# Performance work log

Measured on AMD Instinct MI355X. Metric: run time of the kernel, lower is better.

## Reference

```python
import jax, jax.numpy as jnp
import numpy as np

BLOCK_SIZE = 32
BITS = 4
Q_MAX = 2 ** (BITS - 1) - 1  # 7


def setup_inputs() -> dict:
    key = jax.random.key(0)
    k1, k2, k3, k4 = jax.random.split(key, 4)
    B, S, D_in, D_out = 4, 2048, 4096, 4096
    x = jax.random.normal(k1, (B, S, D_in), dtype=jnp.float32)
    # 4-bit symmetric quantized values in [-8, 7], stored as int32
    weight_q = jax.random.randint(k2, (D_out, D_in), -(2 ** (BITS - 1)), 2 ** (BITS - 1), dtype=jnp.int32)
    # per-block positive scales (abs-max of each block in the original)
    block_scales = jax.random.uniform(k3, (D_out, D_in // BLOCK_SIZE), dtype=jnp.float32, minval=0.01, maxval=1.0)
    bias = jax.random.normal(k4, (D_out,), dtype=jnp.float32) * 0.01
    return {"x": x, "weight_q": weight_q, "block_scales": block_scales, "bias": bias}


def _dequantize(weight_q, block_scales):
    out_f, in_f = weight_q.shape
    n_blocks = in_f // BLOCK_SIZE
    q = weight_q.reshape(out_f, n_blocks, BLOCK_SIZE).astype(jnp.float32)
    w = q / Q_MAX * block_scales[:, :, None]
    return w.reshape(out_f, in_f)


def reference(x, weight_q, block_scales, bias):
    # block dequantize: w = q / q_max * scale, then y = x @ w.T + b
    w = _dequantize(weight_q, block_scales)  # [out, in] fp32
    return jnp.einsum('bsi,oi->bso', x, w) + bias
```

## Files before the change

kernel.cpp:

```cpp
#include <hip/hip_runtime.h>
#include <stdint.h>

#define M_DIM 8192
#define N_DIM 4096
#define K_DIM 4096
#define NBLK  (K_DIM / 32)

typedef __attribute__((ext_vector_type(4))) float          f32x4;
typedef __attribute__((ext_vector_type(8))) short          bf16x8;
typedef __attribute__((ext_vector_type(4))) int            i32x4;
typedef __attribute__((ext_vector_type(8))) unsigned short u16x8;

__device__ __forceinline__ unsigned short f2bf(float f) {
  unsigned u = __builtin_bit_cast(unsigned, f);
  u += 0x7fffu + ((u >> 16) & 1u);
  return (unsigned short)(u >> 16);
}

__device__ __forceinline__ void gload_lds16(const unsigned short* g, unsigned short* l) {
  __builtin_amdgcn_global_load_lds(
      (const __attribute__((address_space(1))) void*)g,
      (__attribute__((address_space(3))) void*)l, 16, 0, 0);
}

__global__ void MXFP4_dequant_kernel(const int* __restrict__ wq,
                                     const float* __restrict__ scales,
                                     unsigned short* __restrict__ wb) {
  int t = blockIdx.x * 256 + threadIdx.x;
  long e = (long)t * 8;
  int o = t >> 9;
  int k = (t & 511) << 3;
  float s = scales[o * NBLK + (k >> 5)] * (1.0f / 7.0f);
  i32x4 q0 = *(const i32x4*)(wq + e);
  i32x4 q1 = *(const i32x4*)(wq + e + 4);
  u16x8 r;
#pragma unroll
  for (int j = 0; j < 4; ++j) r[j]     = f2bf((float)q0[j] * s);
#pragma unroll
  for (int j = 0; j < 4; ++j) r[4 + j] = f2bf((float)q1[j] * s);
  *(u16x8*)(wb + e) = r;
}

__global__ void MXFP4_cvt_kernel(const float* __restrict__ x,
                                 unsigned short* __restrict__ xb) {
  long t = (long)blockIdx.x * 256 + threadIdx.x;
  long e = t * 8;
  f32x4 v0 = *(const f32x4*)(x + e);
  f32x4 v1 = *(const f32x4*)(x + e + 4);
  u16x8 r;
#pragma unroll
  for (int j = 0; j < 4; ++j) r[j]     = f2bf(v0[j]);
#pragma unroll
  for (int j = 0; j < 4; ++j) r[4 + j] = f2bf(v1[j]);
  *(u16x8*)(xb + e) = r;
}

__global__ __launch_bounds__(256, 2) void MXFP4_gemm_kernel(
    const unsigned short* __restrict__ A,
    const unsigned short* __restrict__ B,
    const float* __restrict__ bias,
    float* __restrict__ C) {
  __shared__ unsigned short As[128 * 32];
  __shared__ unsigned short Bs[128 * 32];

  const int tid  = threadIdx.x;
  const int lane = tid & 63;
  const int wave = tid >> 6;
  const int brow = blockIdx.y * 128;
  const int bcol = blockIdx.x * 128;
  const int wm   = (wave >> 1) * 64;
  const int wn   = (wave & 1) * 64;

  const int r0 = tid >> 2;
  const int c0 = (tid & 3) * 8;
  const unsigned short* ag0 = A + (long)(brow + r0) * K_DIM + c0;
  const unsigned short* ag1 = A + (long)(brow + r0 + 64) * K_DIM + c0;
  const unsigned short* bg0 = B + (long)(bcol + r0) * K_DIM + c0;
  const unsigned short* bg1 = B + (long)(bcol + r0 + 64) * K_DIM + c0;
  unsigned short* as0 = As + tid * 8;
  unsigned short* as1 = As + 2048 + tid * 8;
  unsigned short* bs0 = Bs + tid * 8;
  unsigned short* bs1 = Bs + 2048 + tid * 8;

  f32x4 acc[4][4] = {};

  const int fr = lane & 15;
  const int kc = (lane >> 4) * 8;

  for (int kt = 0; kt < K_DIM / 32; ++kt) {
    gload_lds16(ag0, as0);
    gload_lds16(ag1, as1);
    gload_lds16(bg0, bs0);
    gload_lds16(bg1, bs1);
    ag0 += 32; ag1 += 32; bg0 += 32; bg1 += 32;
    __syncthreads();

    bf16x8 af[4], bfr[4];
#pragma unroll
    for (int m = 0; m < 4; ++m)
      af[m] = *(const bf16x8*)(As + (wm + m * 16 + fr) * 32 + kc);
#pragma unroll
    for (int n = 0; n < 4; ++n)
      bfr[n] = *(const bf16x8*)(Bs + (wn + n * 16 + fr) * 32 + kc);
#pragma unroll
    for (int m = 0; m < 4; ++m)
#pragma unroll
      for (int n = 0; n < 4; ++n)
        acc[m][n] = __builtin_amdgcn_mfma_f32_16x16x32_bf16(af[m], bfr[n], acc[m][n], 0, 0, 0);
    __syncthreads();
  }

  const int rbase = brow + wm + (lane >> 4) * 4;
  const int cn    = lane & 15;
#pragma unroll
  for (int n = 0; n < 4; ++n) {
    int col  = bcol + wn + n * 16 + cn;
    float bv = bias[col];
#pragma unroll
    for (int m = 0; m < 4; ++m) {
      int row = rbase + m * 16;
#pragma unroll
      for (int j = 0; j < 4; ++j)
        C[(long)(row + j) * N_DIM + col] = acc[m][n][j] + bv;
    }
  }
}

extern "C" void kernel_launch(void* const* d_in, const int* in_sizes, int n_in,
                              void* d_out, int out_size, void* d_ws, size_t ws_size,
                              hipStream_t stream) {
  const float* x      = (const float*)d_in[0];
  const int*   wq     = (const int*)d_in[1];
  const float* scales = (const float*)d_in[2];
  const float* bias   = (const float*)d_in[3];
  float*       out    = (float*)d_out;

  unsigned short* wb = (unsigned short*)d_ws;
  unsigned short* xb = wb + (size_t)N_DIM * K_DIM;

  MXFP4_dequant_kernel<<<(N_DIM * (long)K_DIM / 8) / 256, 256, 0, stream>>>(wq, scales, wb);
  MXFP4_cvt_kernel<<<(M_DIM * (long)K_DIM / 8) / 256, 256, 0, stream>>>(x, xb);

  dim3 grid(N_DIM / 128, M_DIM / 128);
  MXFP4_gemm_kernel<<<grid, 256, 0, stream>>>(xb, wb, bias, out);
}
```

Before: 365.3 us.

## Rewrite GEMM as 256x256 tile, 8-wave double-buffered pipeline with swizzled grid

Replaces the 128x128 single-buffered bf16 GEMM with a 256x256 tile computed by 512 threads. K steps of 64 are double-buffered in LDS, with global-to-LDS staging interleaved between MFMA quarter-groups, explicit ds_read_b128 via inline asm, manual waitcnt/barrier control and s_setprio around MFMA bursts. The block index is also swizzled for L2 locality. The aim is to hide load latency and raise data reuse per LDS byte, at the cost of more registers, about 130 KB of LDS, and fragile hand-tuned vmcnt accounting.

```diff
diff --git a/kernel.cpp b/kernel.cpp
--- a/kernel.cpp
+++ b/kernel.cpp
@@ -10,6 +10,7 @@
 typedef __attribute__((ext_vector_type(8))) short          bf16x8;
 typedef __attribute__((ext_vector_type(4))) int            i32x4;
 typedef __attribute__((ext_vector_type(8))) unsigned short u16x8;
+typedef __attribute__((address_space(3))) unsigned short   lds_us;
 
 __device__ __forceinline__ unsigned short f2bf(float f) {
   unsigned u = __builtin_bit_cast(unsigned, f);
@@ -17,10 +18,17 @@
   return (unsigned short)(u >> 16);
 }
 
-__device__ __forceinline__ void gload_lds16(const unsigned short* g, unsigned short* l) {
+__device__ __forceinline__ void stage16(const unsigned short* g, lds_us* l) {
   __builtin_amdgcn_global_load_lds(
       (const __attribute__((address_space(1))) void*)g,
       (__attribute__((address_space(3))) void*)l, 16, 0, 0);
+}
+
+template <int OFF>
+__device__ __forceinline__ bf16x8 dsr(lds_us* addr) {
+  bf16x8 d;
+  asm volatile("ds_read_b128 %0, %1 offset:%2" : "=v"(d) : "v"(addr), "n"(OFF));
+  return d;
 }
 
 __global__ void MXFP4_dequant_kernel(const int* __restrict__ wq,
@@ -55,73 +63,139 @@
   *(u16x8*)(xb + e) = r;
 }
 
-__global__ __launch_bounds__(256, 2) void MXFP4_gemm_kernel(
+
+#define BAR() __builtin_amdgcn_s_barrier()
+#define WAIT_LGKM0() do { asm volatile("s_waitcnt lgkmcnt(0)" ::: "memory"); \
+                          __builtin_amdgcn_sched_barrier(0); } while (0)
+
+#define ST_A(t_, h_, BUFA_, valid_) do { \
+  if (valid_) { \
+    const unsigned short* s_ = srcA + (size_t)(h_) * 128 * K_DIM + (t_) * 64; \
+    lds_us* d_ = lp + (BUFA_) * 16384 + ((h_) * 8 + wv) * 1024; \
+    stage16(s_, d_); stage16(s_ + 32, d_ + 512); \
+  } else { stage16(srcA, lp + 65536); stage16(srcA + 32, lp + 65536 + 512); } \
+} while (0)
+
+#define ST_B(t_, h_, BUFB_, valid_) do { \
+  if (valid_) { \
+    const unsigned short* s_ = srcB + (size_t)(h_) * 128 * K_DIM + (t_) * 64; \
+    lds_us* d_ = lp + 32768 + (BUFB_) * 16384 + ((h_) * 8 + wv) * 1024; \
+    stage16(s_, d_); stage16(s_ + 32, d_ + 512); \
+  } else { stage16(srcB, lp + 65536); stage16(srcB + 32, lp + 65536 + 512); } \
+} while (0)
+
+#define MF(MB_, NB_, AF_, BF_) do { \
+  _Pragma("unroll") \
+  for (int kk_ = 0; kk_ < 2; ++kk_) \
+    _Pragma("unroll") \
+    for (int mm_ = 0; mm_ < 4; ++mm_) \
+      _Pragma("unroll") \
+      for (int nn_ = 0; nn_ < 2; ++nn_) \
+        acc[(MB_) + mm_][(NB_) + nn_] = __builtin_amdgcn_mfma_f32_16x16x32_bf16( \
+            AF_[mm_][kk_], BF_[nn_][kk_], acc[(MB_) + mm_][(NB_) + nn_], 0, 0, 0); \
+} while (0)
+
+#define GROUP(BUF_, tB_, tA_, vB_, vA_) do { \
+  lds_us* dsA_ = lp + (BUF_) * 16384 + wm * 8192 + lane * 8; \
+  lds_us* dsB_ = lp + 32768 + (BUF_) * 16384 + wn * 4096 + lane * 8; \
+   \
+  aLo[0][0] = dsr<0>(dsA_);      aLo[0][1] = dsr<1024>(dsA_); \
+  aLo[1][0] = dsr<2048>(dsA_);   aLo[1][1] = dsr<3072>(dsA_); \
+  aLo[2][0] = dsr<4096>(dsA_);   aLo[2][1] = dsr<5120>(dsA_); \
+  aLo[3][0] = dsr<6144>(dsA_);   aLo[3][1] = dsr<7168>(dsA_); \
+  bLo[0][0] = dsr<0>(dsB_);      bLo[0][1] = dsr<1024>(dsB_); \
+  bLo[1][0] = dsr<2048>(dsB_);   bLo[1][1] = dsr<3072>(dsB_); \
+  ST_B(tB_, 0, (BUF_) ^ 1, vB_); \
+  BAR(); WAIT_LGKM0(); \
+  __builtin_amdgcn_s_setprio(1); \
+  MF(0, 0, aLo, bLo); \
+  __builtin_amdgcn_s_setprio(0); \
+  BAR(); \
+   \
+  aHi[0][0] = dsr<8192>(dsA_);   aHi[0][1] = dsr<9216>(dsA_); \
+  aHi[1][0] = dsr<10240>(dsA_);  aHi[1][1] = dsr<11264>(dsA_); \
+  aHi[2][0] = dsr<12288>(dsA_);  aHi[2][1] = dsr<13312>(dsA_); \
+  aHi[3][0] = dsr<14336>(dsA_);  aHi[3][1] = dsr<15360>(dsA_); \
+  ST_B(tB_, 1, (BUF_) ^ 1, vB_); \
+  BAR(); WAIT_LGKM0(); \
+  __builtin_amdgcn_s_setprio(1); \
+  MF(4, 0, aHi, bLo); \
+  __builtin_amdgcn_s_setprio(0); \
+  BAR(); \
+   \
+  bHi[0][0] = dsr<4096>(dsB_);   bHi[0][1] = dsr<5120>(dsB_); \
+  bHi[1][0] = dsr<6144>(dsB_);   bHi[1][1] = dsr<7168>(dsB_); \
+  ST_A(tA_, 0, (BUF_), vA_); \
+  BAR(); WAIT_LGKM0(); \
+  __builtin_amdgcn_s_setprio(1); \
+  MF(0, 2, aLo, bHi); \
+  __builtin_amdgcn_s_setprio(0); \
+  BAR(); \
+   \
+  ST_A(tA_, 1, (BUF_), vA_); \
+  asm volatile("s_waitcnt vmcnt(4)" ::: "memory"); \
+  BAR(); \
+  __builtin_amdgcn_s_setprio(1); \
+  MF(4, 2, aHi, bHi); \
+  __builtin_amdgcn_s_setprio(0); \
+  BAR(); \
+} while (0)
+
+__global__ __launch_bounds__(512, 2) void MXFP4_gemm_kernel(
     const unsigned short* __restrict__ A,
     const unsigned short* __restrict__ B,
     const float* __restrict__ bias,
     float* __restrict__ C) {
-  __shared__ unsigned short As[128 * 32];
-  __shared__ unsigned short Bs[128 * 32];
+  __shared__ unsigned short LDS[66560];
+  lds_us* lp = (lds_us*)LDS;
 
   const int tid  = threadIdx.x;
   const int lane = tid & 63;
-  const int wave = tid >> 6;
-  const int brow = blockIdx.y * 128;
-  const int bcol = blockIdx.x * 128;
-  const int wm   = (wave >> 1) * 64;
-  const int wn   = (wave & 1) * 64;
-
-  const int r0 = tid >> 2;
-  const int c0 = (tid & 3) * 8;
-  const unsigned short* ag0 = A + (long)(brow + r0) * K_DIM + c0;
-  const unsigned short* ag1 = A + (long)(brow + r0 + 64) * K_DIM + c0;
-  const unsigned short* bg0 = B + (long)(bcol + r0) * K_DIM + c0;
-  const unsigned short* bg1 = B + (long)(bcol + r0 + 64) * K_DIM + c0;
-  unsigned short* as0 = As + tid * 8;
-  unsigned short* as1 = As + 2048 + tid * 8;
-  unsigned short* bs0 = Bs + tid * 8;
-  unsigned short* bs1 = Bs + 2048 + tid * 8;
-
-  f32x4 acc[4][4] = {};
-
-  const int fr = lane & 15;
-  const int kc = (lane >> 4) * 8;
-
-  for (int kt = 0; kt < K_DIM / 32; ++kt) {
-    gload_lds16(ag0, as0);
-    gload_lds16(ag1, as1);
-    gload_lds16(bg0, bs0);
-    gload_lds16(bg1, bs1);
-    ag0 += 32; ag1 += 32; bg0 += 32; bg1 += 32;
-    __syncthreads();
-
-    bf16x8 af[4], bfr[4];
-#pragma unroll
-    for (int m = 0; m < 4; ++m)
-      af[m] = *(const bf16x8*)(As + (wm + m * 16 + fr) * 32 + kc);
-#pragma unroll
-    for (int n = 0; n < 4; ++n)
-      bfr[n] = *(const bf16x8*)(Bs + (wn + n * 16 + fr) * 32 + kc);
-#pragma unroll
-    for (int m = 0; m < 4; ++m)
-#pragma unroll
-      for (int n = 0; n < 4; ++n)
-        acc[m][n] = __builtin_amdgcn_mfma_f32_16x16x32_bf16(af[m], bfr[n], acc[m][n], 0, 0, 0);
-    __syncthreads();
+  const int wv   = tid >> 6;
+  const int wm   = wv >> 2;
+  const int wn   = wv & 3;
+
+  const int bid = blockIdx.x;
+  const int sw  = (bid & 7) * 64 + (bid >> 3);
+  const int tn  = sw >> 5;
+  const int tm  = sw & 31;
+  const int brow = tm * 256;
+  const int bcol = tn * 256;
+
+  const unsigned short* srcA =
+      A + (size_t)(brow + wv * 16 + (lane & 15)) * K_DIM + ((lane >> 4) * 8);
+  const unsigned short* srcB =
+      B + (size_t)(bcol + wv * 16 + (lane & 15)) * K_DIM + ((lane >> 4) * 8);
+
+  f32x4 acc[8][4] = {};
+  bf16x8 aLo[4][2], aHi[4][2], bLo[2][2], bHi[2][2];
+
+  ST_A(0, 0, 0, true); ST_A(0, 1, 0, true);
+  ST_B(0, 0, 0, true); ST_B(0, 1, 0, true);
+  ST_A(1, 0, 1, true); ST_A(1, 1, 1, true);
+  asm volatile("s_waitcnt vmcnt(4)" ::: "memory");
+  BAR();
+
+  for (int it = 0; it < 31; ++it) {
+    const int g0 = 2 * it;
+    GROUP(0, g0 + 1, g0 + 2, true, true);
+    GROUP(1, g0 + 2, g0 + 3, true, true);
   }
-
-  const int rbase = brow + wm + (lane >> 4) * 4;
-  const int cn    = lane & 15;
+  GROUP(0, 63, 64, true, false);
+  GROUP(1, 64, 65, false, false);
+
+  const int rb = brow + wm * 128 + (lane >> 4) * 4;
+  const int cb = bcol + wn * 64 + (lane & 15);
 #pragma unroll
   for (int n = 0; n < 4; ++n) {
-    int col  = bcol + wn + n * 16 + cn;
-    float bv = bias[col];
-#pragma unroll
-    for (int m = 0; m < 4; ++m) {
-      int row = rbase + m * 16;
+    const int col = cb + n * 16;
+    const float bv = bias[col];
+#pragma unroll
+    for (int m = 0; m < 8; ++m) {
+      const int row = rb + m * 16;
 #pragma unroll
       for (int j = 0; j < 4; ++j)
-        C[(long)(row + j) * N_DIM + col] = acc[m][n][j] + bv;
+        C[(size_t)(row + j) * N_DIM + col] = acc[m][n][j] + bv;
     }
   }
 }
@@ -141,6 +215,5 @@
   MXFP4_dequant_kernel<<<(N_DIM * (long)K_DIM / 8) / 256, 256, 0, stream>>>(wq, scales, wb);
   MXFP4_cvt_kernel<<<(M_DIM * (long)K_DIM / 8) / 256, 256, 0, stream>>>(x, xb);
 
-  dim3 grid(N_DIM / 128, M_DIM / 128);
-  MXFP4_gemm_kernel<<<grid, 256, 0, stream>>>(xb, wb, bias, out);
-}
+  MXFP4_gemm_kernel<<<512, 512, 0, stream>>>(xb, wb, bias, out);
+}
```

New measurement: 327.7 us. 1.11x faster.
